# Kernel optimization log

Measured on AMD Instinct MI355X. Metric: run time of the kernel, lower is better.

## Reference

```python
import jax, jax.numpy as jnp
import numpy as np

T, B, X, H1, H2 = 512, 256, 256, 256, 256


def setup_inputs() -> dict:
    key = jax.random.key(0)
    ks = jax.random.split(key, 9)
    s = 1.0 / np.sqrt(H1)
    return {
        "a_batch_of_seqs": jax.random.normal(ks[0], (T, B, X), dtype=jnp.float32),
        "initial_state_layer1": jnp.zeros((B, H1), dtype=jnp.float32),
        "initial_state_layer2": jnp.zeros((B, H2), dtype=jnp.float32),
        "W_ih1": jax.random.normal(ks[1], (H1, X), dtype=jnp.float32) * s,
        "W_hh1": jax.random.normal(ks[2], (H1, H1), dtype=jnp.float32) * s,
        "b_ih1": jax.random.normal(ks[3], (H1,), dtype=jnp.float32) * s,
        "b_hh1": jax.random.normal(ks[4], (H1,), dtype=jnp.float32) * s,
        "W_ih2": jax.random.normal(ks[5], (H2, H1), dtype=jnp.float32) * s,
        "W_hh2": jax.random.normal(ks[6], (H2, H2), dtype=jnp.float32) * s,
        "b_ih2": jax.random.normal(ks[7], (H2,), dtype=jnp.float32) * s,
        "b_hh2": jax.random.normal(ks[8], (H2,), dtype=jnp.float32) * s,
    }


def reference(a_batch_of_seqs, initial_state_layer1, initial_state_layer2,
              W_ih1, W_hh1, b_ih1, b_hh1, W_ih2, W_hh2, b_ih2, b_hh2):
    # Precompute input projections for both layers' input-to-hidden of layer1
    # (layer2's input depends on h1, so it stays inside the scan).
    x_proj = jnp.einsum('tbx,hx->tbh', a_batch_of_seqs, W_ih1) + b_ih1  # [T,B,H1]

    def step(carry, xp):
        h1, h2 = carry
        h1 = jnp.tanh(xp + h1 @ W_hh1.T + b_hh1)
        h2 = jnp.tanh(h1 @ W_ih2.T + b_ih2 + h2 @ W_hh2.T + b_hh2)
        return (h1, h2), h2

    (h1_f, h2_f), outputs = jax.lax.scan(step, (initial_state_layer1, initial_state_layer2), x_proj)
    return outputs, h1_f, h2_f
```

## Files before the change

### kernel.cpp

```cpp
#include <hip/hip_runtime.h>


#define TT 512
#define BB 256
#define HH 256
#define LSTR 280

typedef _Float16 f16;
typedef _Float16 f16x8 __attribute__((ext_vector_type(8)));
typedef float f32x4  __attribute__((ext_vector_type(4)));

__device__ inline float tanh_fast(float x) {
    float e = __expf(2.0f * x);
    return 1.0f - 2.0f * __builtin_amdgcn_rcpf(e + 1.0f);
}
__device__ inline void lds_barrier() {
    asm volatile("s_waitcnt lgkmcnt(0)\n\ts_barrier" ::: "memory");
}
__device__ inline void pack_wfrag2h(const float* __restrict__ wrow, f16x8& hi, f16x8& lo) {
    const float4* p = (const float4*)wrow;
    float4 v0 = p[0], v1 = p[1];
    float w[8] = {v0.x, v0.y, v0.z, v0.w, v1.x, v1.y, v1.z, v1.w};
#pragma unroll
    for (int i = 0; i < 8; ++i) {
        f16 h = (f16)w[i];
        hi[i] = h;
        lo[i] = (f16)(w[i] - (float)h);
    }
}
__device__ inline f32x4 mfma16h(f16x8 a, f16x8 b, f32x4 c) {
    return __builtin_amdgcn_mfma_f32_16x16x32_f16(a, b, c, 0, 0, 0);
}

template<bool IN_F16>
__global__ __launch_bounds__(512, 2)
void proj_kernel(const void* __restrict__ Ain, const float* __restrict__ W,
                 const float* __restrict__ bias_a, const float* __restrict__ bias_b,
                 float* __restrict__ Cout)
{
    __shared__ f16 lds_a[64 * LSTR];
    const int tid  = threadIdx.x;
    const int lane = tid & 63, wv = tid >> 6;
    const int quad = lane >> 4, l15 = lane & 15;
    const int n0   = wv * 32;

    f16x8 wh[2][8], wl[2][8];
    float  biasv[2];
#pragma unroll
    for (int nt = 0; nt < 2; ++nt) {
        int n = n0 + nt * 16 + l15;
        biasv[nt] = bias_a[n] + (bias_b ? bias_b[n] : 0.0f);
#pragma unroll
        for (int kc = 0; kc < 8; ++kc)
            pack_wfrag2h(W + (size_t)n * HH + kc * 32 + quad * 8, wh[nt][kc], wl[nt][kc]);
    }

    for (int it = 0; it < 4; ++it) {
        const int m0 = (blockIdx.x * 4 + it) * 64;
        if (IN_F16) {
            const unsigned short* A = (const unsigned short*)Ain;
#pragma unroll
            for (int j = 0; j < 4; ++j) {
                int c = tid + j * 512;
                int row = c >> 5, col8 = c & 31;
                uint4 v = *(const uint4*)(A + (size_t)(m0 + row) * HH + col8 * 8);
                *(uint4*)&lds_a[row * LSTR + col8 * 8] = v;
            }
        } else {
            const float* A = (const float*)Ain;
#pragma unroll
            for (int j = 0; j < 8; ++j) {
                int c = tid + j * 512;
                int row = c >> 6, col4 = c & 63;
                float4 v = *(const float4*)(A + (size_t)(m0 + row) * HH + col4 * 4);
                f16 h0 = (f16)v.x, h1 = (f16)v.y, h2 = (f16)v.z, h3 = (f16)v.w;
                unsigned int p0 = (unsigned int)__builtin_bit_cast(unsigned short, h0) |
                                  ((unsigned int)__builtin_bit_cast(unsigned short, h1) << 16);
                unsigned int p1 = (unsigned int)__builtin_bit_cast(unsigned short, h2) |
                                  ((unsigned int)__builtin_bit_cast(unsigned short, h3) << 16);
                *(uint2*)&lds_a[row * LSTR + col4 * 4] = make_uint2(p0, p1);
            }
        }
        __syncthreads();

        f32x4 acc[4][2];
#pragma unroll
        for (int mt = 0; mt < 4; ++mt)
#pragma unroll
            for (int nt = 0; nt < 2; ++nt)
                acc[mt][nt] = (f32x4){0.f, 0.f, 0.f, 0.f};

#pragma unroll
        for (int kc = 0; kc < 8; ++kc) {
            f16x8 ah[4];
#pragma unroll
            for (int mt = 0; mt < 4; ++mt)
                ah[mt] = *(const f16x8*)&lds_a[(mt * 16 + l15) * LSTR + kc * 32 + quad * 8];
#pragma unroll
            for (int mt = 0; mt < 4; ++mt)
#pragma unroll
                for (int nt = 0; nt < 2; ++nt) {
                    acc[mt][nt] = mfma16h(ah[mt], wh[nt][kc], acc[mt][nt]);
                    acc[mt][nt] = mfma16h(ah[mt], wl[nt][kc], acc[mt][nt]);
                }
        }

#pragma unroll
        for (int mt = 0; mt < 4; ++mt)
#pragma unroll
            for (int nt = 0; nt < 2; ++nt)
#pragma unroll
                for (int r = 0; r < 4; ++r) {
                    int row = m0 + mt * 16 + quad * 4 + r;
                    int col = n0 + nt * 16 + l15;
                    Cout[(size_t)row * HH + col] = acc[mt][nt][r] + biasv[nt];
                }
        __syncthreads();
    }
}

__global__ __launch_bounds__(512, 2)
void scan1_kernel(const float* __restrict__ x1,
                  const float* __restrict__ Whh1,
                  const float* __restrict__ bhh1,
                  const float* __restrict__ h0,
                  f16* __restrict__ h1g,
                  float* __restrict__ h1f)
{
    __shared__ f16 hs[2][16 * LSTR];
    const int tid  = threadIdx.x;
    const int lane = tid & 63, wv = tid >> 6;
    const int quad = lane >> 4, l15 = lane & 15;
    const int m0   = blockIdx.x * 16;
    const int n0   = wv * 32;

    f16x8 wh[2][8], wl[2][8];
    float  biasv[2];
#pragma unroll
    for (int nt = 0; nt < 2; ++nt) {
        int n = n0 + nt * 16 + l15;
        biasv[nt] = bhh1[n];
#pragma unroll
        for (int kc = 0; kc < 8; ++kc)
            pack_wfrag2h(Whh1 + (size_t)n * HH + kc * 32 + quad * 8, wh[nt][kc], wl[nt][kc]);
    }
#pragma unroll
    for (int j = 0; j < 8; ++j) {
        int idx = tid + j * 512;
        int row = idx >> 8, col = idx & 255;
        hs[0][row * LSTR + col] = (f16)h0[(size_t)(m0 + row) * HH + col];
    }
    __syncthreads();

    const int colb = n0 + l15;
    const int rowb = quad * 4;

    float xc[2][4];
#pragma unroll
    for (int nt = 0; nt < 2; ++nt)
#pragma unroll
        for (int r = 0; r < 4; ++r)
            xc[nt][r] = x1[(size_t)(m0 + rowb + r) * HH + colb + nt * 16];

    for (int t = 0; t < TT; ++t) {
        const int cur = t & 1, nxt = (t + 1) & 1;
        const size_t base = ((size_t)t * BB + m0) * HH;
        const int tn = (t + 1 < TT) ? (t + 1) : t;
        const size_t basen = ((size_t)tn * BB + m0) * HH;

        float xn[2][4];
#pragma unroll
        for (int nt = 0; nt < 2; ++nt)
#pragma unroll
            for (int r = 0; r < 4; ++r)
                xn[nt][r] = x1[basen + (size_t)(rowb + r) * HH + colb + nt * 16];

        f32x4 accA[2] = {(f32x4){0.f,0.f,0.f,0.f}, (f32x4){0.f,0.f,0.f,0.f}};
        f32x4 accB[2] = {(f32x4){0.f,0.f,0.f,0.f}, (f32x4){0.f,0.f,0.f,0.f}};
#pragma unroll
        for (int kc = 0; kc < 4; ++kc) {
            const int kd = kc + 4;
            f16x8 ahA = *(const f16x8*)&hs[cur][l15 * LSTR + kc * 32 + quad * 8];
            f16x8 ahB = *(const f16x8*)&hs[cur][l15 * LSTR + kd * 32 + quad * 8];
#pragma unroll
            for (int nt = 0; nt < 2; ++nt) {
                accA[nt] = mfma16h(ahA, wh[nt][kc], accA[nt]);
                accA[nt] = mfma16h(ahA, wl[nt][kc], accA[nt]);
                accB[nt] = mfma16h(ahB, wh[nt][kd], accB[nt]);
                accB[nt] = mfma16h(ahB, wl[nt][kd], accB[nt]);
            }
        }

#pragma unroll
        for (int nt = 0; nt < 2; ++nt) {
            f32x4 acc = accA[nt] + accB[nt];
#pragma unroll
            for (int r = 0; r < 4; ++r) {
                float pre = acc[r] + xc[nt][r] + biasv[nt];
                float h   = tanh_fast(pre);
                f16 hb    = (f16)h;
                int row = rowb + r, col = colb + nt * 16;
                hs[nxt][row * LSTR + col] = hb;
                h1g[base + (size_t)row * HH + col] = hb;
                if (t == TT - 1) h1f[(size_t)(m0 + row) * HH + col] = h;
            }
        }
        lds_barrier();
#pragma unroll
        for (int nt = 0; nt < 2; ++nt)
#pragma unroll
            for (int r = 0; r < 4; ++r)
                xc[nt][r] = xn[nt][r];
    }
}

__global__ __launch_bounds__(512, 2)
void scan2_kernel(float* __restrict__ u,
                  const float* __restrict__ Whh2,
                  const float* __restrict__ h0,
                  float* __restrict__ h2f)
{
    __shared__ f16 hs[2][16 * LSTR];
    const int tid  = threadIdx.x;
    const int lane = tid & 63, wv = tid >> 6;
    const int quad = lane >> 4, l15 = lane & 15;
    const int m0   = blockIdx.x * 16;
    const int n0   = wv * 32;

    f16x8 wh[2][8], wl[2][8];
#pragma unroll
    for (int nt = 0; nt < 2; ++nt) {
        int n = n0 + nt * 16 + l15;
#pragma unroll
        for (int kc = 0; kc < 8; ++kc)
            pack_wfrag2h(Whh2 + (size_t)n * HH + kc * 32 + quad * 8, wh[nt][kc], wl[nt][kc]);
    }
#pragma unroll
    for (int j = 0; j < 8; ++j) {
        int idx = tid + j * 512;
        int row = idx >> 8, col = idx & 255;
        hs[0][row * LSTR + col] = (f16)h0[(size_t)(m0 + row) * HH + col];
    }
    __syncthreads();

    const int colb = n0 + l15;
    const int rowb = quad * 4;

    float uc[2][4];
#pragma unroll
    for (int nt = 0; nt < 2; ++nt)
#pragma unroll
        for (int r = 0; r < 4; ++r)
            uc[nt][r] = u[(size_t)(m0 + rowb + r) * HH + colb + nt * 16];

    for (int t = 0; t < TT; ++t) {
        const int cur = t & 1, nxt = (t + 1) & 1;
        const size_t base = ((size_t)t * BB + m0) * HH;
        const int tn = (t + 1 < TT) ? (t + 1) : t;
        const size_t basen = ((size_t)tn * BB + m0) * HH;

        float un[2][4];
#pragma unroll
        for (int nt = 0; nt < 2; ++nt)
#pragma unroll
            for (int r = 0; r < 4; ++r)
                un[nt][r] = u[basen + (size_t)(rowb + r) * HH + colb + nt * 16];

        f32x4 accA[2] = {(f32x4){0.f,0.f,0.f,0.f}, (f32x4){0.f,0.f,0.f,0.f}};
        f32x4 accB[2] = {(f32x4){0.f,0.f,0.f,0.f}, (f32x4){0.f,0.f,0.f,0.f}};
#pragma unroll
        for (int kc = 0; kc < 4; ++kc) {
            const int kd = kc + 4;
            f16x8 ahA = *(const f16x8*)&hs[cur][l15 * LSTR + kc * 32 + quad * 8];
            f16x8 ahB = *(const f16x8*)&hs[cur][l15 * LSTR + kd * 32 + quad * 8];
#pragma unroll
            for (int nt = 0; nt < 2; ++nt) {
                accA[nt] = mfma16h(ahA, wh[nt][kc], accA[nt]);
                accA[nt] = mfma16h(ahA, wl[nt][kc], accA[nt]);
                accB[nt] = mfma16h(ahB, wh[nt][kd], accB[nt]);
                accB[nt] = mfma16h(ahB, wl[nt][kd], accB[nt]);
            }
        }

#pragma unroll
        for (int nt = 0; nt < 2; ++nt) {
            f32x4 acc = accA[nt] + accB[nt];
#pragma unroll
            for (int r = 0; r < 4; ++r) {
                float pre = acc[r] + uc[nt][r];
                float h   = tanh_fast(pre);
                int row = rowb + r, col = colb + nt * 16;
                hs[nxt][row * LSTR + col] = (f16)h;
                u[base + (size_t)row * HH + col] = h;
                if (t == TT - 1) h2f[(size_t)(m0 + row) * HH + col] = h;
            }
        }
        lds_barrier();
#pragma unroll
        for (int nt = 0; nt < 2; ++nt)
#pragma unroll
            for (int r = 0; r < 4; ++r)
                uc[nt][r] = un[nt][r];
    }
}

extern "C" void kernel_launch(void* const* d_in, const int* in_sizes, int n_in,
                              void* d_out, int out_size, void* d_ws, size_t ws_size,
                              hipStream_t stream)
{
    const float* A     = (const float*)d_in[0];
    const float* is1   = (const float*)d_in[1];
    const float* is2   = (const float*)d_in[2];
    const float* W_ih1 = (const float*)d_in[3];
    const float* W_hh1 = (const float*)d_in[4];
    const float* b_ih1 = (const float*)d_in[5];
    const float* b_hh1 = (const float*)d_in[6];
    const float* W_ih2 = (const float*)d_in[7];
    const float* W_hh2 = (const float*)d_in[8];
    const float* b_ih2 = (const float*)d_in[9];
    const float* b_hh2 = (const float*)d_in[10];

    float* out = (float*)d_out;
    const size_t OUT0 = (size_t)TT * BB * HH;
    float* x1  = out;
    f16*   h1g = (f16*)d_ws;
    float* h1f = out + OUT0;
    float* h2f = out + OUT0 + (size_t)BB * HH;

    proj_kernel<false><<<dim3(512), dim3(512), 0, stream>>>(
        (const void*)A, W_ih1, b_ih1, nullptr, x1);
    scan1_kernel<<<dim3(16), dim3(512), 0, stream>>>(x1, W_hh1, b_hh1, is1, h1g, h1f);
    proj_kernel<true><<<dim3(512), dim3(512), 0, stream>>>(
        (const void*)h1g, W_ih2, b_ih2, b_hh2, out);
    scan2_kernel<<<dim3(16), dim3(512), 0, stream>>>(out, W_hh2, is2, h2f);
}
```

Before: 1.263 ms.

## Fuse both RNN layer scans into one kernel and drop split-f16 weight precision

Merges the layer-1 scan, the layer-2 input projection and the layer-2 scan into a single recurrent kernel. Each step computes h1, then h1@W_ih2 and h2@W_hh2, which removes the second projection launch and the f16 h1 round trip through global memory. It also drops the hi/lo split-f16 weight compensation, halving the MFMA count per product at the cost of accuracy. The fused loop adds a second barrier per step, triples the weight register footprint, and no longer prefetches the next step's input.

```diff
diff --git a/kernel.cpp b/kernel.cpp
--- a/kernel.cpp
+++ b/kernel.cpp
@@ -17,26 +17,21 @@
 __device__ inline void lds_barrier() {
     asm volatile("s_waitcnt lgkmcnt(0)\n\ts_barrier" ::: "memory");
 }
-__device__ inline void pack_wfrag2h(const float* __restrict__ wrow, f16x8& hi, f16x8& lo) {
+__device__ inline f16x8 pack_wfragh(const float* __restrict__ wrow) {
     const float4* p = (const float4*)wrow;
     float4 v0 = p[0], v1 = p[1];
-    float w[8] = {v0.x, v0.y, v0.z, v0.w, v1.x, v1.y, v1.z, v1.w};
-#pragma unroll
-    for (int i = 0; i < 8; ++i) {
-        f16 h = (f16)w[i];
-        hi[i] = h;
-        lo[i] = (f16)(w[i] - (float)h);
-    }
+    f16x8 h;
+    h[0] = (f16)v0.x; h[1] = (f16)v0.y; h[2] = (f16)v0.z; h[3] = (f16)v0.w;
+    h[4] = (f16)v1.x; h[5] = (f16)v1.y; h[6] = (f16)v1.z; h[7] = (f16)v1.w;
+    return h;
 }
 __device__ inline f32x4 mfma16h(f16x8 a, f16x8 b, f32x4 c) {
     return __builtin_amdgcn_mfma_f32_16x16x32_f16(a, b, c, 0, 0, 0);
 }
 
-template<bool IN_F16>
 __global__ __launch_bounds__(512, 2)
-void proj_kernel(const void* __restrict__ Ain, const float* __restrict__ W,
-                 const float* __restrict__ bias_a, const float* __restrict__ bias_b,
-                 float* __restrict__ Cout)
+void proj_kernel(const float* __restrict__ Ain, const float* __restrict__ W,
+                 const float* __restrict__ bias, float* __restrict__ Cout)
 {
     __shared__ f16 lds_a[64 * LSTR];
     const int tid  = threadIdx.x;
@@ -44,42 +39,30 @@
     const int quad = lane >> 4, l15 = lane & 15;
     const int n0   = wv * 32;
 
-    f16x8 wh[2][8], wl[2][8];
-    float  biasv[2];
+    f16x8 wh[2][8];
+    float biasv[2];
 #pragma unroll
     for (int nt = 0; nt < 2; ++nt) {
         int n = n0 + nt * 16 + l15;
-        biasv[nt] = bias_a[n] + (bias_b ? bias_b[n] : 0.0f);
+        biasv[nt] = bias[n];
 #pragma unroll
         for (int kc = 0; kc < 8; ++kc)
-            pack_wfrag2h(W + (size_t)n * HH + kc * 32 + quad * 8, wh[nt][kc], wl[nt][kc]);
+            wh[nt][kc] = pack_wfragh(W + (size_t)n * HH + kc * 32 + quad * 8);
     }
 
     for (int it = 0; it < 4; ++it) {
         const int m0 = (blockIdx.x * 4 + it) * 64;
-        if (IN_F16) {
-            const unsigned short* A = (const unsigned short*)Ain;
-#pragma unroll
-            for (int j = 0; j < 4; ++j) {
-                int c = tid + j * 512;
-                int row = c >> 5, col8 = c & 31;
-                uint4 v = *(const uint4*)(A + (size_t)(m0 + row) * HH + col8 * 8);
-                *(uint4*)&lds_a[row * LSTR + col8 * 8] = v;
-            }
-        } else {
-            const float* A = (const float*)Ain;
-#pragma unroll
-            for (int j = 0; j < 8; ++j) {
-                int c = tid + j * 512;
-                int row = c >> 6, col4 = c & 63;
-                float4 v = *(const float4*)(A + (size_t)(m0 + row) * HH + col4 * 4);
-                f16 h0 = (f16)v.x, h1 = (f16)v.y, h2 = (f16)v.z, h3 = (f16)v.w;
-                unsigned int p0 = (unsigned int)__builtin_bit_cast(unsigned short, h0) |
-                                  ((unsigned int)__builtin_bit_cast(unsigned short, h1) << 16);
-                unsigned int p1 = (unsigned int)__builtin_bit_cast(unsigned short, h2) |
-                                  ((unsigned int)__builtin_bit_cast(unsigned short, h3) << 16);
-                *(uint2*)&lds_a[row * LSTR + col4 * 4] = make_uint2(p0, p1);
-            }
+#pragma unroll
+        for (int j = 0; j < 8; ++j) {
+            int c = tid + j * 512;
+            int row = c >> 6, col4 = c & 63;
+            float4 v = *(const float4*)(Ain + (size_t)(m0 + row) * HH + col4 * 4);
+            f16 h0 = (f16)v.x, h1 = (f16)v.y, h2 = (f16)v.z, h3 = (f16)v.w;
+            unsigned int p0 = (unsigned int)__builtin_bit_cast(unsigned short, h0) |
+                              ((unsigned int)__builtin_bit_cast(unsigned short, h1) << 16);
+            unsigned int p1 = (unsigned int)__builtin_bit_cast(unsigned short, h2) |
+                              ((unsigned int)__builtin_bit_cast(unsigned short, h3) << 16);
+            *(uint2*)&lds_a[row * LSTR + col4 * 4] = make_uint2(p0, p1);
         }
         __syncthreads();
 
@@ -99,10 +82,8 @@
 #pragma unroll
             for (int mt = 0; mt < 4; ++mt)
 #pragma unroll
-                for (int nt = 0; nt < 2; ++nt) {
+                for (int nt = 0; nt < 2; ++nt)
                     acc[mt][nt] = mfma16h(ah[mt], wh[nt][kc], acc[mt][nt]);
-                    acc[mt][nt] = mfma16h(ah[mt], wl[nt][kc], acc[mt][nt]);
-                }
         }
 
 #pragma unroll
@@ -120,187 +101,109 @@
 }
 
 __global__ __launch_bounds__(512, 2)
-void scan1_kernel(const float* __restrict__ x1,
-                  const float* __restrict__ Whh1,
-                  const float* __restrict__ bhh1,
-                  const float* __restrict__ h0,
-                  f16* __restrict__ h1g,
-                  float* __restrict__ h1f)
+void fused_scan_kernel(float* __restrict__ xu,
+                       const float* __restrict__ Whh1,
+                       const float* __restrict__ bhh1,
+                       const float* __restrict__ Wih2,
+                       const float* __restrict__ Whh2,
+                       const float* __restrict__ bih2,
+                       const float* __restrict__ bhh2,
+                       const float* __restrict__ h10,
+                       const float* __restrict__ h20,
+                       float* __restrict__ h1f,
+                       float* __restrict__ h2f)
 {
-    __shared__ f16 hs[2][16 * LSTR];
+    __shared__ f16 hs1[2][16 * LSTR];
+    __shared__ f16 hs2[2][16 * LSTR];
     const int tid  = threadIdx.x;
     const int lane = tid & 63, wv = tid >> 6;
     const int quad = lane >> 4, l15 = lane & 15;
     const int m0   = blockIdx.x * 16;
     const int n0   = wv * 32;
 
-    f16x8 wh[2][8], wl[2][8];
-    float  biasv[2];
+    f16x8 w1[2][8], w2[2][8], w3[2][8];
+    float b1v[2], b2v[2];
 #pragma unroll
     for (int nt = 0; nt < 2; ++nt) {
         int n = n0 + nt * 16 + l15;
-        biasv[nt] = bhh1[n];
-#pragma unroll
-        for (int kc = 0; kc < 8; ++kc)
-            pack_wfrag2h(Whh1 + (size_t)n * HH + kc * 32 + quad * 8, wh[nt][kc], wl[nt][kc]);
+        b1v[nt] = bhh1[n];
+        b2v[nt] = bih2[n] + bhh2[n];
+#pragma unroll
+        for (int kc = 0; kc < 8; ++kc) {
+            w1[nt][kc] = pack_wfragh(Whh1 + (size_t)n * HH + kc * 32 + quad * 8);
+            w2[nt][kc] = pack_wfragh(Wih2 + (size_t)n * HH + kc * 32 + quad * 8);
+            w3[nt][kc] = pack_wfragh(Whh2 + (size_t)n * HH + kc * 32 + quad * 8);
+        }
     }
 #pragma unroll
     for (int j = 0; j < 8; ++j) {
         int idx = tid + j * 512;
         int row = idx >> 8, col = idx & 255;
-        hs[0][row * LSTR + col] = (f16)h0[(size_t)(m0 + row) * HH + col];
+        hs1[0][row * LSTR + col] = (f16)h10[(size_t)(m0 + row) * HH + col];
+        hs2[0][row * LSTR + col] = (f16)h20[(size_t)(m0 + row) * HH + col];
     }
     __syncthreads();
 
     const int colb = n0 + l15;
     const int rowb = quad * 4;
-
-    float xc[2][4];
-#pragma unroll
-    for (int nt = 0; nt < 2; ++nt)
-#pragma unroll
-        for (int r = 0; r < 4; ++r)
-            xc[nt][r] = x1[(size_t)(m0 + rowb + r) * HH + colb + nt * 16];
 
     for (int t = 0; t < TT; ++t) {
         const int cur = t & 1, nxt = (t + 1) & 1;
         const size_t base = ((size_t)t * BB + m0) * HH;
-        const int tn = (t + 1 < TT) ? (t + 1) : t;
-        const size_t basen = ((size_t)tn * BB + m0) * HH;
-
-        float xn[2][4];
+
+        float xc[2][4];
 #pragma unroll
         for (int nt = 0; nt < 2; ++nt)
 #pragma unroll
             for (int r = 0; r < 4; ++r)
-                xn[nt][r] = x1[basen + (size_t)(rowb + r) * HH + colb + nt * 16];
-
-        f32x4 accA[2] = {(f32x4){0.f,0.f,0.f,0.f}, (f32x4){0.f,0.f,0.f,0.f}};
-        f32x4 accB[2] = {(f32x4){0.f,0.f,0.f,0.f}, (f32x4){0.f,0.f,0.f,0.f}};
-#pragma unroll
-        for (int kc = 0; kc < 4; ++kc) {
-            const int kd = kc + 4;
-            f16x8 ahA = *(const f16x8*)&hs[cur][l15 * LSTR + kc * 32 + quad * 8];
-            f16x8 ahB = *(const f16x8*)&hs[cur][l15 * LSTR + kd * 32 + quad * 8];
+                xc[nt][r] = xu[base + (size_t)(rowb + r) * HH + colb + nt * 16];
+
+        f32x4 acc1[2] = {(f32x4){0.f,0.f,0.f,0.f}, (f32x4){0.f,0.f,0.f,0.f}};
+        f32x4 acc3[2] = {(f32x4){0.f,0.f,0.f,0.f}, (f32x4){0.f,0.f,0.f,0.f}};
+#pragma unroll
+        for (int kc = 0; kc < 8; ++kc) {
+            f16x8 a1 = *(const f16x8*)&hs1[cur][l15 * LSTR + kc * 32 + quad * 8];
+            f16x8 a3 = *(const f16x8*)&hs2[cur][l15 * LSTR + kc * 32 + quad * 8];
 #pragma unroll
             for (int nt = 0; nt < 2; ++nt) {
-                accA[nt] = mfma16h(ahA, wh[nt][kc], accA[nt]);
-                accA[nt] = mfma16h(ahA, wl[nt][kc], accA[nt]);
-                accB[nt] = mfma16h(ahB, wh[nt][kd], accB[nt]);
-                accB[nt] = mfma16h(ahB, wl[nt][kd], accB[nt]);
+                acc1[nt] = mfma16h(a1, w1[nt][kc], acc1[nt]);
+                acc3[nt] = mfma16h(a3, w3[nt][kc], acc3[nt]);
             }
         }
 
 #pragma unroll
-        for (int nt = 0; nt < 2; ++nt) {
-            f32x4 acc = accA[nt] + accB[nt];
+        for (int nt = 0; nt < 2; ++nt)
 #pragma unroll
             for (int r = 0; r < 4; ++r) {
-                float pre = acc[r] + xc[nt][r] + biasv[nt];
+                float pre = acc1[nt][r] + xc[nt][r] + b1v[nt];
                 float h   = tanh_fast(pre);
-                f16 hb    = (f16)h;
-                int row = rowb + r, col = colb + nt * 16;
-                hs[nxt][row * LSTR + col] = hb;
-                h1g[base + (size_t)row * HH + col] = hb;
-                if (t == TT - 1) h1f[(size_t)(m0 + row) * HH + col] = h;
+                hs1[nxt][(rowb + r) * LSTR + colb + nt * 16] = (f16)h;
+                if (t == TT - 1)
+                    h1f[(size_t)(m0 + rowb + r) * HH + colb + nt * 16] = h;
             }
-        }
         lds_barrier();
+
+        f32x4 acc2[2] = {(f32x4){0.f,0.f,0.f,0.f}, (f32x4){0.f,0.f,0.f,0.f}};
+#pragma unroll
+        for (int kc = 0; kc < 8; ++kc) {
+            f16x8 a2 = *(const f16x8*)&hs1[nxt][l15 * LSTR + kc * 32 + quad * 8];
+#pragma unroll
+            for (int nt = 0; nt < 2; ++nt)
+                acc2[nt] = mfma16h(a2, w2[nt][kc], acc2[nt]);
+        }
+
 #pragma unroll
         for (int nt = 0; nt < 2; ++nt)
 #pragma unroll
-            for (int r = 0; r < 4; ++r)
-                xc[nt][r] = xn[nt][r];
-    }
-}
-
-__global__ __launch_bounds__(512, 2)
-void scan2_kernel(float* __restrict__ u,
-                  const float* __restrict__ Whh2,
-                  const float* __restrict__ h0,
-                  float* __restrict__ h2f)
-{
-    __shared__ f16 hs[2][16 * LSTR];
-    const int tid  = threadIdx.x;
-    const int lane = tid & 63, wv = tid >> 6;
-    const int quad = lane >> 4, l15 = lane & 15;
-    const int m0   = blockIdx.x * 16;
-    const int n0   = wv * 32;
-
-    f16x8 wh[2][8], wl[2][8];
-#pragma unroll
-    for (int nt = 0; nt < 2; ++nt) {
-        int n = n0 + nt * 16 + l15;
-#pragma unroll
-        for (int kc = 0; kc < 8; ++kc)
-            pack_wfrag2h(Whh2 + (size_t)n * HH + kc * 32 + quad * 8, wh[nt][kc], wl[nt][kc]);
-    }
-#pragma unroll
-    for (int j = 0; j < 8; ++j) {
-        int idx = tid + j * 512;
-        int row = idx >> 8, col = idx & 255;
-        hs[0][row * LSTR + col] = (f16)h0[(size_t)(m0 + row) * HH + col];
-    }
-    __syncthreads();
-
-    const int colb = n0 + l15;
-    const int rowb = quad * 4;
-
-    float uc[2][4];
-#pragma unroll
-    for (int nt = 0; nt < 2; ++nt)
-#pragma unroll
-        for (int r = 0; r < 4; ++r)
-            uc[nt][r] = u[(size_t)(m0 + rowb + r) * HH + colb + nt * 16];
-
-    for (int t = 0; t < TT; ++t) {
-        const int cur = t & 1, nxt = (t + 1) & 1;
-        const size_t base = ((size_t)t * BB + m0) * HH;
-        const int tn = (t + 1 < TT) ? (t + 1) : t;
-        const size_t basen = ((size_t)tn * BB + m0) * HH;
-
-        float un[2][4];
-#pragma unroll
-        for (int nt = 0; nt < 2; ++nt)
-#pragma unroll
-            for (int r = 0; r < 4; ++r)
-                un[nt][r] = u[basen + (size_t)(rowb + r) * HH + colb + nt * 16];
-
-        f32x4 accA[2] = {(f32x4){0.f,0.f,0.f,0.f}, (f32x4){0.f,0.f,0.f,0.f}};
-        f32x4 accB[2] = {(f32x4){0.f,0.f,0.f,0.f}, (f32x4){0.f,0.f,0.f,0.f}};
-#pragma unroll
-        for (int kc = 0; kc < 4; ++kc) {
-            const int kd = kc + 4;
-            f16x8 ahA = *(const f16x8*)&hs[cur][l15 * LSTR + kc * 32 + quad * 8];
-            f16x8 ahB = *(const f16x8*)&hs[cur][l15 * LSTR + kd * 32 + quad * 8];
-#pragma unroll
-            for (int nt = 0; nt < 2; ++nt) {
-                accA[nt] = mfma16h(ahA, wh[nt][kc], accA[nt]);
-                accA[nt] = mfma16h(ahA, wl[nt][kc], accA[nt]);
-                accB[nt] = mfma16h(ahB, wh[nt][kd], accB[nt]);
-                accB[nt] = mfma16h(ahB, wl[nt][kd], accB[nt]);
+            for (int r = 0; r < 4; ++r) {
+                float pre = acc2[nt][r] + acc3[nt][r] + b2v[nt];
+                float h   = tanh_fast(pre);
+                hs2[nxt][(rowb + r) * LSTR + colb + nt * 16] = (f16)h;
+                xu[base + (size_t)(rowb + r) * HH + colb + nt * 16] = h;
+                if (t == TT - 1)
+                    h2f[(size_t)(m0 + rowb + r) * HH + colb + nt * 16] = h;
             }
-        }
-
-#pragma unroll
-        for (int nt = 0; nt < 2; ++nt) {
-            f32x4 acc = accA[nt] + accB[nt];
-#pragma unroll
-            for (int r = 0; r < 4; ++r) {
-                float pre = acc[r] + uc[nt][r];
-                float h   = tanh_fast(pre);
-                int row = rowb + r, col = colb + nt * 16;
-                hs[nxt][row * LSTR + col] = (f16)h;
-                u[base + (size_t)row * HH + col] = h;
-                if (t == TT - 1) h2f[(size_t)(m0 + row) * HH + col] = h;
-            }
-        }
         lds_barrier();
-#pragma unroll
-        for (int nt = 0; nt < 2; ++nt)
-#pragma unroll
-            for (int r = 0; r < 4; ++r)
-                uc[nt][r] = un[nt][r];
     }
 }
 
@@ -323,14 +226,11 @@
     float* out = (float*)d_out;
     const size_t OUT0 = (size_t)TT * BB * HH;
     float* x1  = out;
-    f16*   h1g = (f16*)d_ws;
     float* h1f = out + OUT0;
     float* h2f = out + OUT0 + (size_t)BB * HH;
-
-    proj_kernel<false><<<dim3(512), dim3(512), 0, stream>>>(
-        (const void*)A, W_ih1, b_ih1, nullptr, x1);
-    scan1_kernel<<<dim3(16), dim3(512), 0, stream>>>(x1, W_hh1, b_hh1, is1, h1g, h1f);
-    proj_kernel<true><<<dim3(512), dim3(512), 0, stream>>>(
-        (const void*)h1g, W_ih2, b_ih2, b_hh2, out);
-    scan2_kernel<<<dim3(16), dim3(512), 0, stream>>>(out, W_hh2, is2, h2f);
-}
+    (void)d_ws; (void)ws_size;
+
+    proj_kernel<<<dim3(512), dim3(512), 0, stream>>>(A, W_ih1, b_ih1, x1);
+    fused_scan_kernel<<<dim3(16), dim3(512), 0, stream>>>(
+        x1, W_hh1, b_hh1, W_ih2, W_hh2, b_ih2, b_hh2, is1, is2, h1f, h2f);
+}
```

New measurement: 1.166 ms. 1.08x faster.
